# Kernel optimization log

Measured on AMD Instinct MI355X. Metric: run time of the kernel, lower is better.

## Reference

```python
import jax, jax.numpy as jnp
import numpy as np

B, N, K = 2, 2048, 32
NODE_IN, EDGE_IN, H, DEPTH = 64, 48, 128, 3
SCALE = 30.0
EPS = 1e-6


def _norm(x, g, b):
    # Ingraham-style Normalize: gain*(x-mu)/(std+eps)+bias, unbiased std
    mu = jnp.mean(x, axis=-1, keepdims=True)
    sigma = jnp.std(x, axis=-1, keepdims=True, ddof=1)
    return g * (x - mu) / (sigma + EPS) + b


def _gather_nodes(h, idx):
    # h: [B,N,C], idx: [B,N,K] -> [B,N,K,C]
    b, n, k = idx.shape
    flat = jnp.take_along_axis(h, idx.reshape(b, n * k, 1), axis=1)
    return flat.reshape(b, n, k, h.shape[-1])


def setup_inputs() -> dict:
    key = jax.random.key(0)
    ks = jax.random.split(key, 20)
    xav = lambda k, shp: jax.random.normal(k, shp, jnp.float32) * np.sqrt(2.0 / (shp[-2] + shp[-1]))
    return {
        "V": jax.random.normal(ks[0], (B, N, NODE_IN), jnp.float32),
        "E": jax.random.normal(ks[1], (B, N, K, EDGE_IN), jnp.float32),
        "hS": jax.random.normal(ks[2], (B, N, H), jnp.float32),
        "E_idx": jax.random.randint(ks[3], (B, N, K), 0, N, jnp.int32),
        "mask": jnp.ones((B, N), jnp.float32),
        "Wv_w": xav(ks[4], (NODE_IN, H)), "Wv_b": jnp.zeros((H,), jnp.float32),
        "Wv_g": jnp.ones((H,), jnp.float32), "Wv_b2": jnp.zeros((H,), jnp.float32),
        "We_w": xav(ks[5], (EDGE_IN, H)), "We_b": jnp.zeros((H,), jnp.float32),
        "We_g": jnp.ones((H,), jnp.float32), "We_b2": jnp.zeros((H,), jnp.float32),
        "Lw1": xav(ks[6], (DEPTH, 4 * H, H)), "Lb1": jnp.zeros((DEPTH, H), jnp.float32),
        "Lw2": xav(ks[7], (DEPTH, H, H)), "Lb2": jnp.zeros((DEPTH, H), jnp.float32),
        "Lw3": xav(ks[8], (DEPTH, H, H)), "Lb3": jnp.zeros((DEPTH, H), jnp.float32),
        "Ln_g": jnp.ones((DEPTH, H), jnp.float32), "Ln_b": jnp.zeros((DEPTH, H), jnp.float32),
    }


def reference(V, E, hS, E_idx, mask, Wv_w, Wv_b, Wv_g, Wv_b2, We_w, We_b, We_g, We_b2,
              Lw1, Lb1, Lw2, Lb2, Lw3, Lb3, Ln_g, Ln_b):
    h_v = _norm(V @ Wv_w + Wv_b, Wv_g, Wv_b2)          # [B,N,H]
    h_e = _norm(E @ We_w + We_b, We_g, We_b2)          # [B,N,K,H]
    nei_s = _gather_nodes(hS, E_idx)                   # [B,N,K,H]
    vmask = _gather_nodes(mask[..., None], E_idx)[..., 0]  # [B,N,K]
    h = h_v
    for i in range(DEPTH):
        nei_v = _gather_nodes(h, E_idx)                # [B,N,K,H]
        h_exp = jnp.broadcast_to(h[:, :, None, :], nei_v.shape)
        h_EV = jnp.concatenate([h_exp, nei_v, nei_s, h_e], axis=-1)  # [B,N,K,4H]
        m = jax.nn.relu(h_EV @ Lw1[i] + Lb1[i])
        m = jax.nn.relu(m @ Lw2[i] + Lb2[i])
        m = m @ Lw3[i] + Lb3[i]
        m = m * vmask[..., None]
        dh = jnp.sum(m, axis=-2) / SCALE               # [B,N,H]
        h = _norm(h + dh, Ln_g[i], Ln_b[i])            # dropout = identity (eval)
        h = h * mask[..., None]
    return h
```

## Files before the change

kernel.cpp:

```cpp
#include <hip/hip_runtime.h>
#include <hip/hip_bf16.h>

typedef unsigned short u16;
typedef unsigned int u32;
typedef __attribute__((ext_vector_type(8))) short short8;
typedef __attribute__((ext_vector_type(4))) float float4v;

#define DEV __device__ __forceinline__

constexpr int NN = 2048;
constexpr int BN = 4096;
constexpr int NEDGE = 131072;
constexpr float SCALE_INV = 1.0f / 30.0f;
constexpr float EPS = 1e-6f;

DEV u16 f2bf(float f) {
    u32 u = __float_as_uint(f);
    u32 r = (u + 0x7fffu + ((u >> 16) & 1u)) >> 16;
    return (u16)r;
}
DEV float bf2f(u16 v) { return __uint_as_float(((u32)v) << 16); }

__global__ __launch_bounds__(256, 4) void k_setup(
    const float* __restrict__ V, const float* __restrict__ E,
    const float* __restrict__ hS,
    const float* __restrict__ Vw_w, const float* __restrict__ Vw_b,
    const float* __restrict__ Vw_g, const float* __restrict__ Vw_b2,
    const float* __restrict__ We_w, const float* __restrict__ We_b,
    const float* __restrict__ We_g, const float* __restrict__ We_b2,
    const float* __restrict__ Lw1, const float* __restrict__ Lb1,
    const float* __restrict__ Lw2, const float* __restrict__ Lw3,
    float* __restrict__ hout, u16* __restrict__ he, u16* __restrict__ pack,
    float* __restrict__ P, float* __restrict__ G) {
    __shared__ __align__(16) char sBuf[34816];
    __shared__ float sSum[128 * 5];
    __shared__ float sSq[128 * 5];
    int b = blockIdx.x;
    int t = threadIdx.x;

    if (b < 1024) {
        float* sET = (float*)sBuf;
        u16* sOut = (u16*)sBuf;
        int L = t & 63, w = t >> 6;
        size_t rowbase = (size_t)b * 128;

        const float4v* src4 = (const float4v*)(E + rowbase * 48);
        #pragma unroll
        for (int i = 0; i < 6; i++) {
            int idx4 = t + i * 256;
            int r = idx4 / 12, c4 = (idx4 - r * 12) * 4;
            float4v v = src4[idx4];
            sET[(c4 + 0) * 130 + r] = v[0];
            sET[(c4 + 1) * 130 + r] = v[1];
            sET[(c4 + 2) * 130 + r] = v[2];
            sET[(c4 + 3) * 130 + r] = v[3];
        }
        __syncthreads();

        int wcol = __builtin_amdgcn_readfirstlane(w * 32);
        float4v acc0[8], acc1[8];
        #pragma unroll
        for (int ci = 0; ci < 8; ci++) {
            float4v bb = *(const float4v*)(We_b + wcol + ci * 4);
            acc0[ci] = bb;
            acc1[ci] = bb;
        }
        #pragma unroll 4
        for (int k = 0; k < 48; k++) {
            float2 e = *(const float2*)&sET[k * 130 + 2 * L];
            const float* wK = We_w + k * 128 + wcol;
            #pragma unroll
            for (int ci = 0; ci < 8; ci++) {
                float4v wv = *(const float4v*)(wK + ci * 4);
                acc0[ci] += e.x * wv;
                acc1[ci] += e.y * wv;
            }
        }

        float s0 = 0.f, q0 = 0.f, s1 = 0.f, q1 = 0.f;
        #pragma unroll
        for (int ci = 0; ci < 8; ci++) {
            #pragma unroll
            for (int p = 0; p < 4; p++) {
                float a0 = acc0[ci][p], a1 = acc1[ci][p];
                s0 += a0; q0 += a0 * a0;
                s1 += a1; q1 += a1 * a1;
            }
        }
        sSum[(2 * L) * 5 + w] = s0;     sSq[(2 * L) * 5 + w] = q0;
        sSum[(2 * L + 1) * 5 + w] = s1; sSq[(2 * L + 1) * 5 + w] = q1;
        __syncthreads();

        float fs0 = 0.f, fq0 = 0.f, fs1 = 0.f, fq1 = 0.f;
        #pragma unroll
        for (int j = 0; j < 4; j++) {
            fs0 += sSum[(2 * L) * 5 + j];     fq0 += sSq[(2 * L) * 5 + j];
            fs1 += sSum[(2 * L + 1) * 5 + j]; fq1 += sSq[(2 * L + 1) * 5 + j];
        }
        float mu0 = fs0 * (1.0f / 128.0f), mu1 = fs1 * (1.0f / 128.0f);
        float var0 = (fq0 - 128.0f * mu0 * mu0) * (1.0f / 127.0f);
        float var1 = (fq1 - 128.0f * mu1 * mu1) * (1.0f / 127.0f);
        float inv0 = 1.0f / (sqrtf(var0) + EPS);
        float inv1 = 1.0f / (sqrtf(var1) + EPS);

        u16* out0 = &sOut[(2 * L) * 136 + wcol];
        u16* out1 = &sOut[(2 * L + 1) * 136 + wcol];
        #pragma unroll
        for (int cc = 0; cc < 4; cc++) {
            u32 w0[4], w1[4];
            #pragma unroll
            for (int p = 0; p < 4; p++) {
                int c = cc * 8 + p * 2;
                int ci = c >> 2, pc = c & 3;
                float ga = We_g[wcol + c], gb = We_g[wcol + c + 1];
                float ba = We_b2[wcol + c], bb = We_b2[wcol + c + 1];
                float x0a = ga * (acc0[ci][pc] - mu0) * inv0 + ba;
                float x0b = gb * (acc0[ci][pc + 1] - mu0) * inv0 + bb;
                float x1a = ga * (acc1[ci][pc] - mu1) * inv1 + ba;
                float x1b = gb * (acc1[ci][pc + 1] - mu1) * inv1 + bb;
                w0[p] = (u32)f2bf(x0a) | ((u32)f2bf(x0b) << 16);
                w1[p] = (u32)f2bf(x1a) | ((u32)f2bf(x1b) << 16);
            }
            *(uint4*)(out0 + cc * 8) = make_uint4(w0[0], w0[1], w0[2], w0[3]);
            *(uint4*)(out1 + cc * 8) = make_uint4(w1[0], w1[1], w1[2], w1[3]);
        }
        __syncthreads();

        uint4* dst = (uint4*)(he + rowbase * 128);
        #pragma unroll
        for (int i = 0; i < 8; i++) {
            int c = t + i * 256;
            int row = c >> 4, m = c & 15;
            dst[c] = *(const uint4*)((const char*)sBuf + row * 272 + m * 16);
        }
    } else if (b < 1536) {
        float* sV = (float*)sBuf;
        float* sHn = ((float*)sBuf) + 512;
        float* sSn = ((float*)sBuf) + 1536;
        int nb = (b - 1024) * 8;
        #pragma unroll
        for (int i = 0; i < 2; i++) sV[t + i * 256] = V[(size_t)nb * 64 + t + i * 256];
        #pragma unroll
        for (int i = 0; i < 4; i++) sSn[t + i * 256] = hS[(size_t)nb * 128 + t + i * 256];
        __syncthreads();
        int g = t >> 5, L = t & 31;
        const float* v = &sV[g * 64];
        float a0 = Vw_b[L], a1 = Vw_b[L + 32], a2 = Vw_b[L + 64], a3 = Vw_b[L + 96];
        #pragma unroll 4
        for (int k = 0; k < 64; k++) {
            float vk = v[k];
            const float* wk = Vw_w + k * 128;
            a0 += vk * wk[L];
            a1 += vk * wk[L + 32];
            a2 += vk * wk[L + 64];
            a3 += vk * wk[L + 96];
        }
        float s = a0 + a1 + a2 + a3;
        float q = a0 * a0 + a1 * a1 + a2 * a2 + a3 * a3;
        #pragma unroll
        for (int o = 16; o > 0; o >>= 1) {
            s += __shfl_xor(s, o, 32);
            q += __shfl_xor(q, o, 32);
        }
        float mu = s * (1.0f / 128.0f);
        float var = (q - 128.0f * mu * mu) * (1.0f / 127.0f);
        float inv = 1.0f / (sqrtf(var) + EPS);
        float* outr = hout + (size_t)(nb + g) * 128;
        float o0 = Vw_g[L]      * (a0 - mu) * inv + Vw_b2[L];
        float o1 = Vw_g[L + 32] * (a1 - mu) * inv + Vw_b2[L + 32];
        float o2 = Vw_g[L + 64] * (a2 - mu) * inv + Vw_b2[L + 64];
        float o3 = Vw_g[L + 96] * (a3 - mu) * inv + Vw_b2[L + 96];
        outr[L] = o0; outr[L + 32] = o1; outr[L + 64] = o2; outr[L + 96] = o3;
        sHn[g * 128 + L] = o0;      sHn[g * 128 + L + 32] = o1;
        sHn[g * 128 + L + 64] = o2; sHn[g * 128 + L + 96] = o3;
        __syncthreads();
        int c = t & 127, pr = t >> 7;
        float p[4], gq[4];
        float b1 = Lb1[c];
        #pragma unroll
        for (int i = 0; i < 4; i++) { p[i] = b1; gq[i] = 0.f; }
        #pragma unroll 2
        for (int k = 0; k < 128; k++) {
            float wa = Lw1[k * 128 + c];
            float wb = Lw1[(128 + k) * 128 + c];
            float wc = Lw1[(256 + k) * 128 + c];
            #pragma unroll
            for (int i = 0; i < 4; i++) {
                float hk = sHn[(pr * 4 + i) * 128 + k];
                float sk = sSn[(pr * 4 + i) * 128 + k];
                p[i] += hk * wa;
                gq[i] += hk * wb + sk * wc;
            }
        }
        #pragma unroll
        for (int i = 0; i < 4; i++) {
            P[(size_t)(nb + pr * 4 + i) * 128 + c] = p[i];
            G[(size_t)(nb + pr * 4 + i) * 128 + c] = gq[i];
        }
    } else {
        int lm = b - 1536;
        const float* src;
        if (lm < 6) {
            int l = lm >> 1, mat = lm & 1;
            src = (mat == 0) ? (Lw1 + ((size_t)l * 512 + 384) * 128)
                             : (Lw2 + (size_t)l * 16384);
        } else if (lm < 12) {
            int idx = lm - 6, ll = idx / 3, mi = idx - ll * 3;
            src = Lw1 + (((size_t)(ll + 1) * 512) + mi * 128) * 128;
        } else {
            src = Lw3 + (size_t)(lm - 12) * 16384;
        }
        u16* dst = pack + (size_t)lm * 16384;
        for (int i = 0; i < 64; i++) {
            int idx = t * 64 + i;
            int j = idx & 7, lane = (idx >> 3) & 63, s = (idx >> 9) & 3, tt = idx >> 11;
            int k = s * 32 + (lane >> 4) * 8 + j;
            int n = tt * 16 + (lane & 15);
            dst[idx] = f2bf(src[k * 128 + n]);
        }
    }
}

__global__ __launch_bounds__(256, 3) void k_edge_mlp(
    const u16* __restrict__ he, const float* __restrict__ Pcur,
    const float* __restrict__ Gcur, float* __restrict__ Pnext, float* __restrict__ Gnext,
    const int* __restrict__ Eidx, const float* __restrict__ maskp,
    const u16* __restrict__ pack, const float* __restrict__ Lb2,
    const float* __restrict__ Lb3,
    const float* __restrict__ Lng, const float* __restrict__ Lnb,
    const float* __restrict__ Lb1, const float* __restrict__ hS, int l,
    float* __restrict__ h, float* __restrict__ outp, int last) {
    __shared__ __align__(16) u16 sA[128 * 136];
    __shared__ __align__(16) u16 sHhi[4 * 136];
    __shared__ __align__(16) u16 sHlo[4 * 136];
    __shared__ __align__(16) u16 sShi[4 * 136];
    __shared__ __align__(16) u16 sSlo[4 * 136];
    __shared__ __align__(16) u16 sMhi[16 * 136];
    __shared__ __align__(16) u16 sMlo[16 * 136];
    __shared__ int sJ[128];
    __shared__ float sVm[128];
    __shared__ float sP[4 * 128];
    __shared__ float sM[4 * 128];
    __shared__ float sMs[4];
    __shared__ float sredS[4][2];
    __shared__ float sredQ[4][2];
    int nb = blockIdx.x * 4;
    int t = threadIdx.x;

    for (int i = 4 * 136 + t; i < 16 * 136; i += 256) {
        sMhi[i] = 0;
        sMlo[i] = 0;
    }
    #pragma unroll
    for (int i = 0; i < 2; i++) {
        int idx = t + i * 256;
        int r = idx >> 7, c = idx & 127;
        float x = hS[(size_t)(nb + r) * 128 + c];
        u16 hb = f2bf(x);
        sShi[r * 136 + c] = hb;
        sSlo[r * 136 + c] = f2bf(x - bf2f(hb));
    }

    if (t < 128) {
        int gr = nb + (t >> 5);
        int j = Eidx[nb * 32 + t];
        int jg = (gr >> 11) * NN + j;
        sJ[t] = jg;
        sVm[t] = maskp[jg];
    }
    sP[t] = Pcur[(size_t)nb * 128 + t];
    sP[t + 256] = Pcur[(size_t)nb * 128 + 256 + t];
    {
        const uint4* src = (const uint4*)(he + (size_t)nb * 32 * 128);
        #pragma unroll
        for (int i = 0; i < 8; i++) {
            int idx = i * 256 + t;
            int row = idx >> 4, col = idx & 15;
            *(uint4*)(&sA[row * 136 + col * 8]) = src[idx];
        }
    }
    __syncthreads();

    if (t < 4) {
        float s = 0.f;
        #pragma unroll
        for (int e = 0; e < 32; e++) s += sVm[t * 32 + e];
        sMs[t] = s;
    }

    int w = t >> 6, lane = t & 63, q = lane >> 4, c16 = lane & 15;

    float gv[8][2][4];
    #pragma unroll
    for (int tm = 0; tm < 8; tm++)
        #pragma unroll
        for (int tn = 0; tn < 2; tn++) {
            int n = (2 * w + tn) * 16 + c16;
            #pragma unroll
            for (int r = 0; r < 4; r++) {
                int m = tm * 16 + q * 4 + r;
                gv[tm][tn][r] = Gcur[(size_t)sJ[m] * 128 + n];
            }
        }
    int cpost = t & 127, pr = t >> 7;
    int gr0 = nb + 2 * pr, gr1 = gr0 + 1;
    float h0 = h[(size_t)gr0 * 128 + cpost];
    float h1 = h[(size_t)gr1 * 128 + cpost];

    short8 Bf[2][4];
    const short8* pk1 = (const short8*)(pack + (size_t)(l * 2) * 16384);
    #pragma unroll
    for (int tn = 0; tn < 2; tn++)
        #pragma unroll
        for (int s = 0; s < 4; s++)
            Bf[tn][s] = pk1[((2 * w + tn) * 4 + s) * 64 + lane];

    float4v acc[8][2];
    #pragma unroll
    for (int tm = 0; tm < 8; tm++)
        #pragma unroll
        for (int tn = 0; tn < 2; tn++) acc[tm][tn] = (float4v){0.f, 0.f, 0.f, 0.f};

    #pragma unroll
    for (int tm = 0; tm < 8; tm++) {
        short8 a[4];
        #pragma unroll
        for (int s = 0; s < 4; s++)
            a[s] = *(const short8*)(&sA[(tm * 16 + c16) * 136 + s * 32 + q * 8]);
        #pragma unroll
        for (int s = 0; s < 4; s++) {
            acc[tm][0] = __builtin_amdgcn_mfma_f32_16x16x32_bf16(a[s], Bf[0][s], acc[tm][0], 0, 0, 0);
            acc[tm][1] = __builtin_amdgcn_mfma_f32_16x16x32_bf16(a[s], Bf[1][s], acc[tm][1], 0, 0, 0);
        }
    }
    __syncthreads();

    #pragma unroll
    for (int tm = 0; tm < 8; tm++) {
        #pragma unroll
        for (int tn = 0; tn < 2; tn++) {
            int n = (2 * w + tn) * 16 + c16;
            #pragma unroll
            for (int r = 0; r < 4; r++) {
                int m = tm * 16 + q * 4 + r;
                int g = m >> 5;
                float v = acc[tm][tn][r] + sP[g * 128 + n] + gv[tm][tn][r];
                v = v > 0.f ? v : 0.f;
                sA[m * 136 + n] = f2bf(v);
            }
        }
    }
    __syncthreads();

    const short8* pk2 = (const short8*)(pack + (size_t)(l * 2 + 1) * 16384);
    #pragma unroll
    for (int tn = 0; tn < 2; tn++)
        #pragma unroll
        for (int s = 0; s < 4; s++)
            Bf[tn][s] = pk2[((2 * w + tn) * 4 + s) * 64 + lane];
    #pragma unroll
    for (int tm = 0; tm < 8; tm++)
        #pragma unroll
        for (int tn = 0; tn < 2; tn++) acc[tm][tn] = (float4v){0.f, 0.f, 0.f, 0.f};
    #pragma unroll
    for (int tm = 0; tm < 8; tm++) {
        short8 a[4];
        #pragma unroll
        for (int s = 0; s < 4; s++)
            a[s] = *(const short8*)(&sA[(tm * 16 + c16) * 136 + s * 32 + q * 8]);
        #pragma unroll
        for (int s = 0; s < 4; s++) {
            acc[tm][0] = __builtin_amdgcn_mfma_f32_16x16x32_bf16(a[s], Bf[0][s], acc[tm][0], 0, 0, 0);
            acc[tm][1] = __builtin_amdgcn_mfma_f32_16x16x32_bf16(a[s], Bf[1][s], acc[tm][1], 0, 0, 0);
        }
    }

    float b2v0 = Lb2[l * 128 + (2 * w) * 16 + c16];
    float b2v1 = Lb2[l * 128 + (2 * w + 1) * 16 + c16];
    #pragma unroll
    for (int g = 0; g < 4; g++) {
        float p0 = 0.f, p1 = 0.f;
        #pragma unroll
        for (int half = 0; half < 2; half++) {
            int tm = 2 * g + half;
            #pragma unroll
            for (int r = 0; r < 4; r++) {
                int m = tm * 16 + q * 4 + r;
                float vm = sVm[m];
                float x0 = acc[tm][0][r] + b2v0; x0 = x0 > 0.f ? x0 : 0.f;
                float x1 = acc[tm][1][r] + b2v1; x1 = x1 > 0.f ? x1 : 0.f;
                p0 += vm * x0;
                p1 += vm * x1;
            }
        }
        p0 += __shfl_xor(p0, 16, 64); p0 += __shfl_xor(p0, 32, 64);
        p1 += __shfl_xor(p1, 16, 64); p1 += __shfl_xor(p1, 32, 64);
        if (lane < 32) {
            float val = (lane < 16) ? p0 : p1;
            int col = 32 * w + (lane & 31);
            u16 hb = f2bf(val);
            sMhi[g * 136 + col] = hb;
            sMlo[g * 136 + col] = f2bf(val - bf2f(hb));
        }
    }
    __syncthreads();

    {
        const short8* pk3 = (const short8*)(pack + (size_t)(12 + l) * 16384);
        float4v accW[2];
        accW[0] = (float4v){0.f, 0.f, 0.f, 0.f};
        accW[1] = (float4v){0.f, 0.f, 0.f, 0.f};
        #pragma unroll
        for (int s = 0; s < 4; s++) {
            int off = c16 * 136 + s * 32 + q * 8;
            short8 aMh = *(const short8*)&sMhi[off];
            short8 aMl = *(const short8*)&sMlo[off];
            #pragma unroll
            for (int tn = 0; tn < 2; tn++) {
                int bi = ((2 * w + tn) * 4 + s) * 64 + lane;
                short8 bW = pk3[bi];
                accW[tn] = __builtin_amdgcn_mfma_f32_16x16x32_bf16(aMl, bW, accW[tn], 0, 0, 0);
                accW[tn] = __builtin_amdgcn_mfma_f32_16x16x32_bf16(aMh, bW, accW[tn], 0, 0, 0);
            }
        }
        if (lane < 16) {
            #pragma unroll
            for (int tn = 0; tn < 2; tn++) {
                int col = (2 * w + tn) * 16 + lane;
                #pragma unroll
                for (int r = 0; r < 4; r++) sM[r * 128 + col] = accW[tn][r];
            }
        }
    }
    __syncthreads();

    int c = cpost;
    int g0 = 2 * pr, g1 = g0 + 1;
    float b3 = Lb3[l * 128 + c];
    float gg = Lng[l * 128 + c];
    float bn = Lnb[l * 128 + c];
    float x0 = h0 + (sM[g0 * 128 + c] + sMs[g0] * b3) * SCALE_INV;
    float x1 = h1 + (sM[g1 * 128 + c] + sMs[g1] * b3) * SCALE_INV;
    float s0 = x0, s1 = x1, q0 = x0 * x0, q1 = x1 * x1;
    #pragma unroll
    for (int o = 32; o > 0; o >>= 1) {
        s0 += __shfl_xor(s0, o, 64); q0 += __shfl_xor(q0, o, 64);
        s1 += __shfl_xor(s1, o, 64); q1 += __shfl_xor(q1, o, 64);
    }
    if (lane == 0) {
        sredS[w][0] = s0; sredS[w][1] = s1;
        sredQ[w][0] = q0; sredQ[w][1] = q1;
    }
    __syncthreads();
    int wb = 2 * pr;
    float S0 = sredS[wb][0] + sredS[wb + 1][0];
    float S1 = sredS[wb][1] + sredS[wb + 1][1];
    float Q0 = sredQ[wb][0] + sredQ[wb + 1][0];
    float Q1 = sredQ[wb][1] + sredQ[wb + 1][1];
    float mu0 = S0 * (1.0f / 128.0f), mu1 = S1 * (1.0f / 128.0f);
    float var0 = (Q0 - 128.0f * mu0 * mu0) * (1.0f / 127.0f);
    float var1 = (Q1 - 128.0f * mu1 * mu1) * (1.0f / 127.0f);
    float m0 = maskp[gr0], m1v = maskp[gr1];
    float o0 = (gg * (x0 - mu0) / (sqrtf(var0) + EPS) + bn) * m0;
    float o1 = (gg * (x1 - mu1) / (sqrtf(var1) + EPS) + bn) * m1v;
    h[(size_t)gr0 * 128 + c] = o0;
    h[(size_t)gr1 * 128 + c] = o1;
    if (last) {
        outp[(size_t)gr0 * 128 + c] = o0;
        outp[(size_t)gr1 * 128 + c] = o1;
        return;
    }

    {
        u16 hb0 = f2bf(o0);
        sHhi[g0 * 136 + c] = hb0;
        sHlo[g0 * 136 + c] = f2bf(o0 - bf2f(hb0));
        u16 hb1 = f2bf(o1);
        sHhi[g1 * 136 + c] = hb1;
        sHlo[g1 * 136 + c] = f2bf(o1 - bf2f(hb1));
    }
    __syncthreads();
    {
        const short8* pkA = (const short8*)(pack + (size_t)(6 + l * 3 + 0) * 16384);
        const short8* pkB = (const short8*)(pack + (size_t)(6 + l * 3 + 1) * 16384);
        const short8* pkC = (const short8*)(pack + (size_t)(6 + l * 3 + 2) * 16384);
        float4v accP[2], accG[2];
        #pragma unroll
        for (int tn = 0; tn < 2; tn++) {
            accP[tn] = (float4v){0.f, 0.f, 0.f, 0.f};
            accG[tn] = (float4v){0.f, 0.f, 0.f, 0.f};
        }
        short8 z8 = (short8){0, 0, 0, 0, 0, 0, 0, 0};
        #pragma unroll
        for (int s = 0; s < 4; s++) {
            short8 aHh = z8, aHl = z8, aSh = z8, aSl = z8;
            if (c16 < 4) {
                int off = c16 * 136 + s * 32 + q * 8;
                aHh = *(const short8*)&sHhi[off];
                aHl = *(const short8*)&sHlo[off];
                aSh = *(const short8*)&sShi[off];
                aSl = *(const short8*)&sSlo[off];
            }
            #pragma unroll
            for (int tn = 0; tn < 2; tn++) {
                int bi = ((2 * w + tn) * 4 + s) * 64 + lane;
                short8 bA = pkA[bi], bB = pkB[bi], bC = pkC[bi];
                accP[tn] = __builtin_amdgcn_mfma_f32_16x16x32_bf16(aHl, bA, accP[tn], 0, 0, 0);
                accP[tn] = __builtin_amdgcn_mfma_f32_16x16x32_bf16(aHh, bA, accP[tn], 0, 0, 0);
                accG[tn] = __builtin_amdgcn_mfma_f32_16x16x32_bf16(aHl, bB, accG[tn], 0, 0, 0);
                accG[tn] = __builtin_amdgcn_mfma_f32_16x16x32_bf16(aHh, bB, accG[tn], 0, 0, 0);
                accG[tn] = __builtin_amdgcn_mfma_f32_16x16x32_bf16(aSl, bC, accG[tn], 0, 0, 0);
                accG[tn] = __builtin_amdgcn_mfma_f32_16x16x32_bf16(aSh, bC, accG[tn], 0, 0, 0);
            }
        }
        if (lane < 16) {
            #pragma unroll
            for (int tn = 0; tn < 2; tn++) {
                int col = (2 * w + tn) * 16 + lane;
                float b1v = Lb1[(l + 1) * 128 + col];
                #pragma unroll
                for (int r = 0; r < 4; r++) {
                    Pnext[(size_t)(nb + r) * 128 + col] = accP[tn][r] + b1v;
                    Gnext[(size_t)(nb + r) * 128 + col] = accG[tn][r];
                }
            }
        }
    }
}

extern "C" void kernel_launch(void* const* d_in, const int* in_sizes, int n_in,
                              void* d_out, int out_size, void* d_ws, size_t ws_size,
                              hipStream_t stream) {
    const float* V     = (const float*)d_in[0];
    const float* E     = (const float*)d_in[1];
    const float* hS    = (const float*)d_in[2];
    const int*   Eidx  = (const int*)d_in[3];
    const float* maskp = (const float*)d_in[4];
    const float* Wv_w  = (const float*)d_in[5];
    const float* Wv_b  = (const float*)d_in[6];
    const float* Wv_g  = (const float*)d_in[7];
    const float* Wv_b2 = (const float*)d_in[8];
    const float* We_w  = (const float*)d_in[9];
    const float* We_b  = (const float*)d_in[10];
    const float* We_g  = (const float*)d_in[11];
    const float* We_b2 = (const float*)d_in[12];
    const float* Lw1   = (const float*)d_in[13];
    const float* Lb1   = (const float*)d_in[14];
    const float* Lw2   = (const float*)d_in[15];
    const float* Lb2   = (const float*)d_in[16];
    const float* Lw3   = (const float*)d_in[17];
    const float* Lb3   = (const float*)d_in[18];
    const float* Ln_g  = (const float*)d_in[19];
    const float* Ln_b  = (const float*)d_in[20];

    char* ws = (char*)d_ws;
    float* h    = (float*)ws; ws += (size_t)BN * 128 * 4;
    float* P0   = (float*)ws; ws += (size_t)BN * 128 * 4;
    float* G0   = (float*)ws; ws += (size_t)BN * 128 * 4;
    float* P1   = (float*)ws; ws += (size_t)BN * 128 * 4;
    float* G1   = (float*)ws; ws += (size_t)BN * 128 * 4;
    u16*   he   = (u16*)ws;   ws += (size_t)NEDGE * 128 * 2;
    u16*   pack = (u16*)ws;   ws += (size_t)15 * 16384 * 2;

    k_setup<<<1551, 256, 0, stream>>>(V, E, hS, Wv_w, Wv_b, Wv_g, Wv_b2,
                                      We_w, We_b, We_g, We_b2, Lw1, Lb1, Lw2, Lw3,
                                      h, he, pack, P0, G0);
    for (int l = 0; l < 3; l++) {
        const float* Pc = (l & 1) ? P1 : P0;
        const float* Gc = (l & 1) ? G1 : G0;
        float* Pn = (l & 1) ? P0 : P1;
        float* Gn = (l & 1) ? G0 : G1;
        k_edge_mlp<<<BN / 4, 256, 0, stream>>>(he, Pc, Gc, Pn, Gn,
                                               Eidx, maskp, pack, Lb2,
                                               Lb3, Ln_g, Ln_b, Lb1, hS, l,
                                               h, (float*)d_out, l == 2);
    }
}
```

Baseline: 240.0 us.

## Fuse edge embedding projection and normalization into first-layer edge MLP kernel

```diff
diff --git a/kernel.cpp b/kernel.cpp
--- a/kernel.cpp
+++ b/kernel.cpp
@@ -22,122 +22,22 @@
 DEV float bf2f(u16 v) { return __uint_as_float(((u32)v) << 16); }
 
 __global__ __launch_bounds__(256, 4) void k_setup(
-    const float* __restrict__ V, const float* __restrict__ E,
-    const float* __restrict__ hS,
+    const float* __restrict__ V, const float* __restrict__ hS,
     const float* __restrict__ Vw_w, const float* __restrict__ Vw_b,
     const float* __restrict__ Vw_g, const float* __restrict__ Vw_b2,
-    const float* __restrict__ We_w, const float* __restrict__ We_b,
-    const float* __restrict__ We_g, const float* __restrict__ We_b2,
     const float* __restrict__ Lw1, const float* __restrict__ Lb1,
     const float* __restrict__ Lw2, const float* __restrict__ Lw3,
-    float* __restrict__ hout, u16* __restrict__ he, u16* __restrict__ pack,
+    float* __restrict__ hout, u16* __restrict__ pack,
     float* __restrict__ P, float* __restrict__ G) {
-    __shared__ __align__(16) char sBuf[34816];
-    __shared__ float sSum[128 * 5];
-    __shared__ float sSq[128 * 5];
+    __shared__ __align__(16) float sBuf[2560];
     int b = blockIdx.x;
     int t = threadIdx.x;
 
-    if (b < 1024) {
-        float* sET = (float*)sBuf;
-        u16* sOut = (u16*)sBuf;
-        int L = t & 63, w = t >> 6;
-        size_t rowbase = (size_t)b * 128;
-
-        const float4v* src4 = (const float4v*)(E + rowbase * 48);
-        #pragma unroll
-        for (int i = 0; i < 6; i++) {
-            int idx4 = t + i * 256;
-            int r = idx4 / 12, c4 = (idx4 - r * 12) * 4;
-            float4v v = src4[idx4];
-            sET[(c4 + 0) * 130 + r] = v[0];
-            sET[(c4 + 1) * 130 + r] = v[1];
-            sET[(c4 + 2) * 130 + r] = v[2];
-            sET[(c4 + 3) * 130 + r] = v[3];
-        }
-        __syncthreads();
-
-        int wcol = __builtin_amdgcn_readfirstlane(w * 32);
-        float4v acc0[8], acc1[8];
-        #pragma unroll
-        for (int ci = 0; ci < 8; ci++) {
-            float4v bb = *(const float4v*)(We_b + wcol + ci * 4);
-            acc0[ci] = bb;
-            acc1[ci] = bb;
-        }
-        #pragma unroll 4
-        for (int k = 0; k < 48; k++) {
-            float2 e = *(const float2*)&sET[k * 130 + 2 * L];
-            const float* wK = We_w + k * 128 + wcol;
-            #pragma unroll
-            for (int ci = 0; ci < 8; ci++) {
-                float4v wv = *(const float4v*)(wK + ci * 4);
-                acc0[ci] += e.x * wv;
-                acc1[ci] += e.y * wv;
-            }
-        }
-
-        float s0 = 0.f, q0 = 0.f, s1 = 0.f, q1 = 0.f;
-        #pragma unroll
-        for (int ci = 0; ci < 8; ci++) {
-            #pragma unroll
-            for (int p = 0; p < 4; p++) {
-                float a0 = acc0[ci][p], a1 = acc1[ci][p];
-                s0 += a0; q0 += a0 * a0;
-                s1 += a1; q1 += a1 * a1;
-            }
-        }
-        sSum[(2 * L) * 5 + w] = s0;     sSq[(2 * L) * 5 + w] = q0;
-        sSum[(2 * L + 1) * 5 + w] = s1; sSq[(2 * L + 1) * 5 + w] = q1;
-        __syncthreads();
-
-        float fs0 = 0.f, fq0 = 0.f, fs1 = 0.f, fq1 = 0.f;
-        #pragma unroll
-        for (int j = 0; j < 4; j++) {
-            fs0 += sSum[(2 * L) * 5 + j];     fq0 += sSq[(2 * L) * 5 + j];
-            fs1 += sSum[(2 * L + 1) * 5 + j]; fq1 += sSq[(2 * L + 1) * 5 + j];
-        }
-        float mu0 = fs0 * (1.0f / 128.0f), mu1 = fs1 * (1.0f / 128.0f);
-        float var0 = (fq0 - 128.0f * mu0 * mu0) * (1.0f / 127.0f);
-        float var1 = (fq1 - 128.0f * mu1 * mu1) * (1.0f / 127.0f);
-        float inv0 = 1.0f / (sqrtf(var0) + EPS);
-        float inv1 = 1.0f / (sqrtf(var1) + EPS);
-
-        u16* out0 = &sOut[(2 * L) * 136 + wcol];
-        u16* out1 = &sOut[(2 * L + 1) * 136 + wcol];
-        #pragma unroll
-        for (int cc = 0; cc < 4; cc++) {
-            u32 w0[4], w1[4];
-            #pragma unroll
-            for (int p = 0; p < 4; p++) {
-                int c = cc * 8 + p * 2;
-                int ci = c >> 2, pc = c & 3;
-                float ga = We_g[wcol + c], gb = We_g[wcol + c + 1];
-                float ba = We_b2[wcol + c], bb = We_b2[wcol + c + 1];
-                float x0a = ga * (acc0[ci][pc] - mu0) * inv0 + ba;
-                float x0b = gb * (acc0[ci][pc + 1] - mu0) * inv0 + bb;
-                float x1a = ga * (acc1[ci][pc] - mu1) * inv1 + ba;
-                float x1b = gb * (acc1[ci][pc + 1] - mu1) * inv1 + bb;
-                w0[p] = (u32)f2bf(x0a) | ((u32)f2bf(x0b) << 16);
-                w1[p] = (u32)f2bf(x1a) | ((u32)f2bf(x1b) << 16);
-            }
-            *(uint4*)(out0 + cc * 8) = make_uint4(w0[0], w0[1], w0[2], w0[3]);
-            *(uint4*)(out1 + cc * 8) = make_uint4(w1[0], w1[1], w1[2], w1[3]);
-        }
-        __syncthreads();
-
-        uint4* dst = (uint4*)(he + rowbase * 128);
-        #pragma unroll
-        for (int i = 0; i < 8; i++) {
-            int c = t + i * 256;
-            int row = c >> 4, m = c & 15;
-            dst[c] = *(const uint4*)((const char*)sBuf + row * 272 + m * 16);
-        }
-    } else if (b < 1536) {
-        float* sV = (float*)sBuf;
-        float* sHn = ((float*)sBuf) + 512;
-        float* sSn = ((float*)sBuf) + 1536;
-        int nb = (b - 1024) * 8;
+    if (b < 512) {
+        float* sV = sBuf;
+        float* sHn = sBuf + 512;
+        float* sSn = sBuf + 1536;
+        int nb = b * 8;
         #pragma unroll
         for (int i = 0; i < 2; i++) sV[t + i * 256] = V[(size_t)nb * 64 + t + i * 256];
         #pragma unroll
@@ -198,7 +98,7 @@
             G[(size_t)(nb + pr * 4 + i) * 128 + c] = gq[i];
         }
     } else {
-        int lm = b - 1536;
+        int lm = b - 512;
         const float* src;
         if (lm < 6) {
             int l = lm >> 1, mat = lm & 1;
@@ -222,7 +122,10 @@
 }
 
 __global__ __launch_bounds__(256, 3) void k_edge_mlp(
-    const u16* __restrict__ he, const float* __restrict__ Pcur,
+    const float* __restrict__ E,
+    const float* __restrict__ We_w, const float* __restrict__ We_b,
+    const float* __restrict__ We_g, const float* __restrict__ We_b2,
+    u16* __restrict__ he, const float* __restrict__ Pcur,
     const float* __restrict__ Gcur, float* __restrict__ Pnext, float* __restrict__ Gnext,
     const int* __restrict__ Eidx, const float* __restrict__ maskp,
     const u16* __restrict__ pack, const float* __restrict__ Lb2,
@@ -246,10 +149,13 @@
     __shared__ float sredQ[4][2];
     int nb = blockIdx.x * 4;
     int t = threadIdx.x;
-
-    for (int i = 4 * 136 + t; i < 16 * 136; i += 256) {
-        sMhi[i] = 0;
-        sMlo[i] = 0;
+    int w = t >> 6, lane = t & 63, q = lane >> 4, c16 = lane & 15;
+
+    if (l != 0) {
+        for (int i = 4 * 136 + t; i < 16 * 136; i += 256) {
+            sMhi[i] = 0;
+            sMlo[i] = 0;
+        }
     }
     #pragma unroll
     for (int i = 0; i < 2; i++) {
@@ -270,7 +176,20 @@
     }
     sP[t] = Pcur[(size_t)nb * 128 + t];
     sP[t + 256] = Pcur[(size_t)nb * 128 + 256 + t];
-    {
+    if (l == 0) {
+        float* sET = (float*)sA;
+        const float4v* src4 = (const float4v*)(E + (size_t)blockIdx.x * 128 * 48);
+        #pragma unroll
+        for (int i = 0; i < 6; i++) {
+            int idx4 = t + i * 256;
+            int r = idx4 / 12, c4 = (idx4 - r * 12) * 4;
+            float4v v = src4[idx4];
+            sET[(c4 + 0) * 130 + r] = v[0];
+            sET[(c4 + 1) * 130 + r] = v[1];
+            sET[(c4 + 2) * 130 + r] = v[2];
+            sET[(c4 + 3) * 130 + r] = v[3];
+        }
+    } else {
         const uint4* src = (const uint4*)(he + (size_t)nb * 32 * 128);
         #pragma unroll
         for (int i = 0; i < 8; i++) {
@@ -288,7 +207,90 @@
         sMs[t] = s;
     }
 
-    int w = t >> 6, lane = t & 63, q = lane >> 4, c16 = lane & 15;
+    if (l == 0) {
+        float* sET = (float*)sA;
+        float* sSum = (float*)sMhi;
+        float* sSq = (float*)sMlo;
+        float* sMu = sM;
+        int L = lane;
+        int wcol = __builtin_amdgcn_readfirstlane(w * 32);
+        float4v acc0[8], acc1[8];
+        #pragma unroll
+        for (int ci = 0; ci < 8; ci++) {
+            float4v bb = *(const float4v*)(We_b + wcol + ci * 4);
+            acc0[ci] = bb;
+            acc1[ci] = bb;
+        }
+        #pragma unroll 4
+        for (int k = 0; k < 48; k++) {
+            float2 e = *(const float2*)&sET[k * 130 + 2 * L];
+            const float* wK = We_w + k * 128 + wcol;
+            #pragma unroll
+            for (int ci = 0; ci < 8; ci++) {
+                float4v wv = *(const float4v*)(wK + ci * 4);
+                acc0[ci] += e.x * wv;
+                acc1[ci] += e.y * wv;
+            }
+        }
+        float s0 = 0.f, q0 = 0.f, s1 = 0.f, q1 = 0.f;
+        #pragma unroll
+        for (int ci = 0; ci < 8; ci++) {
+            #pragma unroll
+            for (int p = 0; p < 4; p++) {
+                float a0 = acc0[ci][p], a1 = acc1[ci][p];
+                s0 += a0; q0 += a0 * a0;
+                s1 += a1; q1 += a1 * a1;
+            }
+        }
+        sSum[(2 * L) * 5 + w] = s0;     sSq[(2 * L) * 5 + w] = q0;
+        sSum[(2 * L + 1) * 5 + w] = s1; sSq[(2 * L + 1) * 5 + w] = q1;
+        __syncthreads();
+        if (t < 128) {
+            float fs = 0.f, fq = 0.f;
+            #pragma unroll
+            for (int j = 0; j < 4; j++) { fs += sSum[t * 5 + j]; fq += sSq[t * 5 + j]; }
+            float mu = fs * (1.0f / 128.0f);
+            float var = (fq - 128.0f * mu * mu) * (1.0f / 127.0f);
+            sMu[t] = mu;
+            sMu[128 + t] = 1.0f / (sqrtf(var) + EPS);
+        }
+        __syncthreads();
+        float mu0 = sMu[2 * L], inv0 = sMu[128 + 2 * L];
+        float mu1 = sMu[2 * L + 1], inv1 = sMu[128 + 2 * L + 1];
+        u16* out0 = &sA[(2 * L) * 136 + wcol];
+        u16* out1 = &sA[(2 * L + 1) * 136 + wcol];
+        #pragma unroll
+        for (int cc = 0; cc < 4; cc++) {
+            u32 w0[4], w1[4];
+            #pragma unroll
+            for (int p = 0; p < 4; p++) {
+                int c = cc * 8 + p * 2;
+                int ci = c >> 2, pc = c & 3;
+                float ga = We_g[wcol + c], gb = We_g[wcol + c + 1];
+                float ba = We_b2[wcol + c], bb = We_b2[wcol + c + 1];
+                float x0a = ga * (acc0[ci][pc] - mu0) * inv0 + ba;
+                float x0b = gb * (acc0[ci][pc + 1] - mu0) * inv0 + bb;
+                float x1a = ga * (acc1[ci][pc] - mu1) * inv1 + ba;
+                float x1b = gb * (acc1[ci][pc + 1] - mu1) * inv1 + bb;
+                w0[p] = (u32)f2bf(x0a) | ((u32)f2bf(x0b) << 16);
+                w1[p] = (u32)f2bf(x1a) | ((u32)f2bf(x1b) << 16);
+            }
+            *(uint4*)(out0 + cc * 8) = make_uint4(w0[0], w0[1], w0[2], w0[3]);
+            *(uint4*)(out1 + cc * 8) = make_uint4(w1[0], w1[1], w1[2], w1[3]);
+        }
+        for (int i = 4 * 136 + t; i < 16 * 136; i += 256) {
+            sMhi[i] = 0;
+            sMlo[i] = 0;
+        }
+        __syncthreads();
+        uint4* dst = (uint4*)(he + (size_t)blockIdx.x * 128 * 128);
+        #pragma unroll
+        for (int i = 0; i < 8; i++) {
+            int c = t + i * 256;
+            int row = c >> 4, m = c & 15;
+            dst[c] = *(const uint4*)((const char*)sA + row * 272 + m * 16);
+        }
+    }
 
     float gv[8][2][4];
     #pragma unroll
@@ -423,6 +425,7 @@
                 accW[tn] = __builtin_amdgcn_mfma_f32_16x16x32_bf16(aMh, bW, accW[tn], 0, 0, 0);
             }
         }
+        __syncthreads();
         if (lane < 16) {
             #pragma unroll
             for (int tn = 0; tn < 2; tn++) {
@@ -562,15 +565,15 @@
     u16*   he   = (u16*)ws;   ws += (size_t)NEDGE * 128 * 2;
     u16*   pack = (u16*)ws;   ws += (size_t)15 * 16384 * 2;
 
-    k_setup<<<1551, 256, 0, stream>>>(V, E, hS, Wv_w, Wv_b, Wv_g, Wv_b2,
-                                      We_w, We_b, We_g, We_b2, Lw1, Lb1, Lw2, Lw3,
-                                      h, he, pack, P0, G0);
+    k_setup<<<527, 256, 0, stream>>>(V, hS, Wv_w, Wv_b, Wv_g, Wv_b2,
+                                     Lw1, Lb1, Lw2, Lw3, h, pack, P0, G0);
     for (int l = 0; l < 3; l++) {
         const float* Pc = (l & 1) ? P1 : P0;
         const float* Gc = (l & 1) ? G1 : G0;
         float* Pn = (l & 1) ? P0 : P1;
         float* Gn = (l & 1) ? G0 : G1;
-        k_edge_mlp<<<BN / 4, 256, 0, stream>>>(he, Pc, Gc, Pn, Gn,
+        k_edge_mlp<<<BN / 4, 256, 0, stream>>>(E, We_w, We_b, We_g, We_b2,
+                                               he, Pc, Gc, Pn, Gn,
                                                Eidx, maskp, pack, Lb2,
                                                Lb3, Ln_g, Ln_b, Lb1, hS, l,
                                                h, (float*)d_out, l == 2);
```

New measurement: 289.4 us. 20.6% more time.
